# Kernel tuning notes

Measured on AMD Instinct MI355X. Metric: run time of the kernel, lower is better.

Reference implementation:

```python
import jax, jax.numpy as jnp
import numpy as np

N, E, H = 4096, 32768, 8
D0, C1, C2, C3 = 256, 448, 384, 256
K, M, G = 4, 500, 2000
NEG = 0.2   # GATConv LeakyReLU negative slope
EPS = 1e-5  # LayerNorm eps


def _gat(x, src, dst, W, a_s, a_d, b, heads, out_ch, concat):
    # PyG GATConv (self-loops already appended to src/dst by caller).
    n = x.shape[0]
    xp = (x @ W).reshape(n, heads, out_ch)                 # [N,H,C]
    s = jnp.einsum('nhc,hc->nh', xp, a_s)                  # alpha_src per node
    d = jnp.einsum('nhc,hc->nh', xp, a_d)                  # alpha_dst per node
    e = jax.nn.leaky_relu(s[src] + d[dst], NEG)            # [E,H]
    m = jax.ops.segment_max(e, dst, num_segments=n)
    m = jnp.where(jnp.isfinite(m), m, 0.0)
    p = jnp.exp(e - m[dst])
    z = jax.ops.segment_sum(p, dst, num_segments=n)
    alpha = p / (z[dst] + 1e-16)                           # per-dst softmax
    out = jax.ops.segment_sum(alpha[:, :, None] * xp[src], dst, num_segments=n)
    out = out.reshape(n, heads * out_ch) if concat else out[:, 0, :]
    return out + b


def _ln(x, g, b):
    mu = x.mean(-1, keepdims=True)
    v = ((x - mu) ** 2).mean(-1, keepdims=True)
    return (x - mu) * jax.lax.rsqrt(v + EPS) * g + b


def setup_inputs() -> dict:
    key = jax.random.key(0)
    ks = jax.random.split(key, 20)
    sc = 0.05
    inp = {
        'x': jax.random.normal(ks[0], (N, D0), jnp.float32),
        'edge_index': jax.random.randint(ks[1], (2, E), 0, N, jnp.int32),
        'W1': jax.random.normal(ks[2], (D0, H * C1), jnp.float32) * sc,
        'as1': jax.random.normal(ks[3], (H, C1), jnp.float32) * sc,
        'ad1': jax.random.normal(ks[4], (H, C1), jnp.float32) * sc,
        'b1': jnp.zeros((H * C1,), jnp.float32),
        'g1': jnp.ones((H * C1,), jnp.float32),
        'be1': jnp.zeros((H * C1,), jnp.float32),
        'W2': jax.random.normal(ks[5], (H * C1, H * C2), jnp.float32) * sc,
        'as2': jax.random.normal(ks[6], (H, C2), jnp.float32) * sc,
        'ad2': jax.random.normal(ks[7], (H, C2), jnp.float32) * sc,
        'b2': jnp.zeros((H * C2,), jnp.float32),
        'g2': jnp.ones((H * C2,), jnp.float32),
        'be2': jnp.zeros((H * C2,), jnp.float32),
        'W3': jax.random.normal(ks[8], (H * C2, H * C3), jnp.float32) * sc,
        'as3': jax.random.normal(ks[9], (H, C3), jnp.float32) * sc,
        'ad3': jax.random.normal(ks[10], (H, C3), jnp.float32) * sc,
        'b3': jnp.zeros((H * C3,), jnp.float32),
        'g3': jnp.ones((H * C3,), jnp.float32),
        'be3': jnp.zeros((H * C3,), jnp.float32),
        'Wh': jax.random.normal(ks[11], (K, H * C3, M), jnp.float32) * sc,
        'ash': jax.random.normal(ks[12], (K, 1, M), jnp.float32) * sc,
        'adh': jax.random.normal(ks[13], (K, 1, M), jnp.float32) * sc,
        'bh': jnp.zeros((K, M), jnp.float32),
        'idx': jnp.arange(G, dtype=jnp.int32).reshape(K, M),
    }
    return inp


def reference(x, edge_index, W1, as1, ad1, b1, g1, be1, W2, as2, ad2, b2, g2, be2,
              W3, as3, ad3, b3, g3, be3, Wh, ash, adh, bh, idx):
    n = x.shape[0]
    # eval mode: dropout_edge is identity; PyG GATConv adds self-loops
    loops = jnp.arange(n, dtype=edge_index.dtype)
    src = jnp.concatenate([edge_index[0], loops])
    dst = jnp.concatenate([edge_index[1], loops])

    h = jax.nn.relu(_gat(x, src, dst, W1, as1, ad1, b1, H, C1, True))
    h = _ln(h, g1, be1)
    h = jax.nn.relu(_gat(h, src, dst, W2, as2, ad2, b2, H, C2, True))
    h = _ln(h, g2, be2)
    h = jax.nn.relu(_gat(h, src, dst, W3, as3, ad3, b3, H, C3, True))
    h = _ln(h, g3, be3)

    per_head = jax.vmap(
        lambda Wk, ak_s, ak_d, bk: _gat(h, src, dst, Wk, ak_s, ak_d, bk, 1, M, False)
    )(Wh, ash, adh, bh)                                    # [K,N,M]

    vals = per_head.transpose(1, 0, 2).reshape(n, K * M)   # [N, G] in head order
    full = jnp.zeros((n, G), vals.dtype).at[:, idx.reshape(-1)].set(vals)
    return full, per_head
```

## Files before the change

### kernel.cpp

```cpp
#include <hip/hip_runtime.h>

#define NN 4096
#define EE 32768
#define ETOT (EE + NN)
#define HH 8
#define KK 4
#define MM 500
#define GG 2000
#define NEGS 0.2f
#define LNEPS 1e-5f

typedef unsigned short ushort;
typedef _Float16 half_t;
typedef __attribute__((ext_vector_type(8))) _Float16 half8;
typedef __attribute__((ext_vector_type(4))) _Float16 half4;
typedef __attribute__((ext_vector_type(4))) float floatx4;


__device__ __forceinline__ void get_edge(const int* __restrict__ ei, int e, int& s, int& d) {
    if (e < EE) { s = ei[e]; d = ei[EE + e]; }
    else        { s = e - EE; d = e - EE; }
}

__device__ __forceinline__ half_t f2h(float x) { return (half_t)x; }

__device__ __forceinline__ void async_lds16(const half_t* g, half_t* l) {
    __builtin_amdgcn_global_load_lds(
        (const __attribute__((address_space(1))) unsigned int*)(const void*)g,
        (__attribute__((address_space(3))) unsigned int*)(void*)l,
        16, 0, 0);
}


__global__ void k_count(const int* __restrict__ ei, int* deg) {
    int e = blockIdx.x * 256 + threadIdx.x;
    if (e < ETOT) { int s, d; get_edge(ei, e, s, d); atomicAdd(&deg[d], 1); }
}

__global__ void k_scan(int* deg, int* rs, int n) {
    __shared__ int sums[1024];
    int tid = threadIdx.x;
    int base = tid * 4;
    int loc[4]; int s = 0;
    #pragma unroll
    for (int i = 0; i < 4; i++) {
        int v = (base + i < n) ? deg[base + i] : 0;
        loc[i] = s; s += v;
    }
    #pragma unroll
    for (int i = 0; i < 4; i++)
        if (base + i < n) deg[base + i] = 0;
    sums[tid] = s;
    __syncthreads();
    for (int off = 1; off < 1024; off <<= 1) {
        int v = (tid >= off) ? sums[tid - off] : 0;
        __syncthreads();
        sums[tid] += v;
        __syncthreads();
    }
    int prev = (tid > 0) ? sums[tid - 1] : 0;
    #pragma unroll
    for (int i = 0; i < 4; i++)
        if (base + i < n) rs[base + i] = prev + loc[i];
    if (tid == 1023) rs[n] = sums[1023];
}

__global__ void k_fill_f2h(const int* __restrict__ ei, const int* __restrict__ rs,
                           int* cur, int* csr_src,
                           const floatx4* __restrict__ x4, half4* __restrict__ xh4) {
    int i = blockIdx.x * 256 + threadIdx.x;
    if (i < ETOT) {
        int s, d; get_edge(ei, i, s, d);
        int pos = rs[d] + atomicAdd(&cur[d], 1);
        csr_src[pos] = s;
    }
    if (i < NN * 64) {
        floatx4 v = x4[i];
        half4 o;
        o[0] = f2h(v[0]); o[1] = f2h(v[1]); o[2] = f2h(v[2]); o[3] = f2h(v[3]);
        xh4[i] = o;
    }
}


__global__ __launch_bounds__(256) void k_wa(const float* __restrict__ W1,
                                            const float* __restrict__ as_,
                                            const float* __restrict__ ad_,
                                            float* was, float* wad, int C, int ldw) {
    int pair = blockIdx.x * 4 + (threadIdx.x >> 6);
    int lane = threadIdx.x & 63;
    int h = pair >> 8, k = pair & 255;
    const float* wrow = W1 + (size_t)k * ldw + (size_t)h * C;
    const float* av = as_ + (size_t)h * C;
    const float* bv = ad_ + (size_t)h * C;
    float ss = 0.f, dd = 0.f;
    for (int c = lane; c < C; c += 64) {
        float w = wrow[c];
        ss += w * av[c];
        dd += w * bv[c];
    }
    #pragma unroll
    for (int o = 32; o > 0; o >>= 1) {
        ss += __shfl_down(ss, o, 64);
        dd += __shfl_down(dd, o, 64);
    }
    if (lane == 0) { was[pair] = ss; wad[pair] = dd; }
}


__global__ __launch_bounds__(256) void k_sd_x(const float* __restrict__ x,
                                              const float* __restrict__ was,
                                              const float* __restrict__ wad,
                                              float* s, float* d) {
    int n = blockIdx.x * 4 + (threadIdx.x >> 6);
    int lane = threadIdx.x & 63;
    const float* xr = x + (size_t)n * 256;
    float x0 = xr[lane], x1 = xr[lane + 64], x2 = xr[lane + 128], x3 = xr[lane + 192];
    #pragma unroll
    for (int h = 0; h < HH; h++) {
        const float* ws = was + h * 256;
        const float* wd = wad + h * 256;
        float ss = x0 * ws[lane] + x1 * ws[lane + 64] + x2 * ws[lane + 128] + x3 * ws[lane + 192];
        float dd = x0 * wd[lane] + x1 * wd[lane + 64] + x2 * wd[lane + 128] + x3 * wd[lane + 192];
        #pragma unroll
        for (int o = 32; o > 0; o >>= 1) {
            ss += __shfl_down(ss, o, 64);
            dd += __shfl_down(dd, o, 64);
        }
        if (lane == 0) { s[n * HH + h] = ss; d[n * HH + h] = dd; }
    }
}


__global__ __launch_bounds__(256) void k_agg_x(
    const half_t* __restrict__ xh, const float* __restrict__ s, const float* __restrict__ d,
    const int* __restrict__ csr_src, const int* __restrict__ rs,
    half_t* __restrict__ aggx) {
    __shared__ half_t sx[16][256];
    __shared__ int ssrc[16];
    __shared__ float sw[16][HH];
    __shared__ float sh_d[HH];
    __shared__ float sh_z[HH];
    int n = blockIdx.x, tid = threadIdx.x;
    int h = tid >> 5, kc = (tid & 31) * 8;
    if (tid < HH) { sh_d[tid] = d[(size_t)n * HH + tid]; sh_z[tid] = 0.f; }
    float acc[8];
    #pragma unroll
    for (int e = 0; e < 8; e++) acc[e] = 0.f;
    int start = rs[n], end = rs[n + 1];

    for (int e0 = start; e0 < end; e0 += 16) {
        int cnt = min(16, end - e0);
        if (tid < cnt) ssrc[tid] = csr_src[e0 + tid];
        __syncthreads();
        for (int q = tid; q < cnt * 32; q += 256) {
            int er = q >> 5, ec = q & 31;
            *((half8*)&sx[er][0] + ec) = *((const half8*)(xh + (size_t)ssrc[er] * 256) + ec);
        }
        if (tid < cnt * HH) {
            int er = tid >> 3, hh = tid & 7;
            float v = s[(size_t)ssrc[er] * HH + hh] + sh_d[hh];
            v = (v >= 0.f) ? v : NEGS * v;
            sw[er][hh] = expf(v);
        }
        __syncthreads();
        if (tid < HH) {
            float zz = 0.f;
            for (int i = 0; i < cnt; i++) zz += sw[i][tid];
            sh_z[tid] += zz;
        }
        for (int i = 0; i < cnt; i++) {
            float w = sw[i][h];
            half8 v = *(const half8*)&sx[i][kc];
            acc[0] += w * (float)v[0]; acc[1] += w * (float)v[1];
            acc[2] += w * (float)v[2]; acc[3] += w * (float)v[3];
            acc[4] += w * (float)v[4]; acc[5] += w * (float)v[5];
            acc[6] += w * (float)v[6]; acc[7] += w * (float)v[7];
        }
    }
    __syncthreads();
    float zi = 1.f / (sh_z[h] + 1e-16f);
    half8 o;
    #pragma unroll
    for (int e = 0; e < 8; e++) o[e] = f2h(acc[e] * zi);
    *(half8*)(aggx + (size_t)n * (HH * 256) + h * 256 + kc) = o;
}


__global__ __launch_bounds__(256) void k_ln(const half_t* __restrict__ xin,
                                            const float* __restrict__ bias,
                                            const float* __restrict__ gam,
                                            const float* __restrict__ bet,
                                            half_t* __restrict__ outh, int Dout) {
    __shared__ float red[256];
    __shared__ float red2[256];
    int n = blockIdx.x, tid = threadIdx.x;
    int NCH = Dout >> 3;
    float vals[2][8];
    float sum = 0.f, sumsq = 0.f;
    int ai = 0;
    for (int ch = tid; ch < NCH; ch += 256, ai++) {
        half8 v = *(const half8*)(xin + (size_t)n * Dout + (ch << 3));
        #pragma unroll
        for (int e = 0; e < 8; e++) {
            float val = (float)v[e] + bias[(ch << 3) + e];
            val = fmaxf(val, 0.f);
            vals[ai][e] = val;
            sum += val; sumsq += val * val;
        }
    }
    red[tid] = sum; red2[tid] = sumsq;
    __syncthreads();
    for (int o = 128; o > 0; o >>= 1) {
        if (tid < o) { red[tid] += red[tid + o]; red2[tid] += red2[tid + o]; }
        __syncthreads();
    }
    float mu = red[0] / Dout;
    float var = red2[0] / Dout - mu * mu;
    float rstd = rsqrtf(var + LNEPS);
    ai = 0;
    for (int ch = tid; ch < NCH; ch += 256, ai++) {
        half8 o;
        #pragma unroll
        for (int e = 0; e < 8; e++)
            o[e] = f2h((vals[ai][e] - mu) * rstd * gam[(ch << 3) + e] + bet[(ch << 3) + e]);
        *(half8*)(outh + (size_t)n * Dout + (ch << 3)) = o;
    }
}


__device__ __forceinline__ void sd_body(const half_t* __restrict__ xp,
                                        const float* __restrict__ as_,
                                        const float* __restrict__ ad_,
                                        float* s, float* d, int H, int C,
                                        int idx, int lane) {
    const half4* row4 = (const half4*)(xp + (size_t)idx * C);
    int h = idx % H;
    const float* av = as_ + (size_t)h * C;
    const float* bv = ad_ + (size_t)h * C;
    int C4 = C >> 2;
    float ss = 0.f, dd = 0.f;
    for (int c4 = lane; c4 < C4; c4 += 64) {
        half4 v = row4[c4];
        floatx4 a = *(const floatx4*)(av + c4 * 4);
        floatx4 b = *(const floatx4*)(bv + c4 * 4);
        float x0 = (float)v[0], x1 = (float)v[1], x2 = (float)v[2], x3 = (float)v[3];
        ss += x0 * a[0] + x1 * a[1] + x2 * a[2] + x3 * a[3];
        dd += x0 * b[0] + x1 * b[1] + x2 * b[2] + x3 * b[3];
    }
    #pragma unroll
    for (int o = 32; o > 0; o >>= 1) {
        ss += __shfl_down(ss, o, 64);
        dd += __shfl_down(dd, o, 64);
    }
    if (lane == 0) { s[idx] = ss; d[idx] = dd; }
}

__global__ __launch_bounds__(256) void k_sd4(const half_t* __restrict__ xp,
                                             const float* __restrict__ as_,
                                             const float* __restrict__ ad_,
                                             float* s, float* d, int H, int C, int npairs) {
    int idx = blockIdx.x * 4 + (threadIdx.x >> 6);
    if (idx < npairs)
        sd_body(xp, as_, ad_, s, d, H, C, idx, threadIdx.x & 63);
}


__global__ __launch_bounds__(256) void k_sd_wt(
    const half_t* __restrict__ xp, const float* __restrict__ as_,
    const float* __restrict__ ad_, float* s, float* d, int H, int C, int nsd, int npairs,
    const float* __restrict__ W, half_t* __restrict__ Wt,
    int Kd, int Nvalid, int ldw, long long sW, long long sWt, int wgx, int wgy) {
    __shared__ float t[32][33];
    int bid = blockIdx.x;
    if (bid < nsd) {
        int idx = bid * 4 + (threadIdx.x >> 6);
        if (idx < npairs)
            sd_body(xp, as_, ad_, s, d, H, C, idx, threadIdx.x & 63);
        return;
    }
    int wb = bid - nsd;
    int bx = wb % wgx;
    int rem = wb / wgx;
    int by = rem % wgy;
    int bz = rem / wgy;
    const float* Wp = W + (size_t)bz * sW;
    half_t* Wtp = Wt + (size_t)bz * sWt;
    int n0 = bx * 32, k0 = by * 32;
    int tx = threadIdx.x & 31, ty = threadIdx.x >> 5;
    #pragma unroll
    for (int i = 0; i < 32; i += 8)
        t[ty + i][tx] = (n0 + tx < Nvalid) ? Wp[(size_t)(k0 + ty + i) * ldw + n0 + tx] : 0.f;
    __syncthreads();
    #pragma unroll
    for (int i = 0; i < 32; i += 8)
        Wtp[(size_t)(n0 + ty + i) * Kd + k0 + tx] = f2h(t[tx][ty + i]);
}


__global__ __launch_bounds__(256) void k_wt(const float* __restrict__ W,
                                            half_t* __restrict__ Wt,
                                            int Kd, int Nvalid, int ldw,
                                            long long sW, long long sWt) {
    __shared__ float t[32][33];
    const float* Wp = W + (size_t)blockIdx.z * sW;
    half_t* Wtp = Wt + (size_t)blockIdx.z * sWt;
    int n0 = blockIdx.x * 32, k0 = blockIdx.y * 32;
    int tx = threadIdx.x & 31, ty = threadIdx.x >> 5;
    #pragma unroll
    for (int i = 0; i < 32; i += 8)
        t[ty + i][tx] = (n0 + tx < Nvalid) ? Wp[(size_t)(k0 + ty + i) * ldw + n0 + tx] : 0.f;
    __syncthreads();
    #pragma unroll
    for (int i = 0; i < 32; i += 8)
        Wtp[(size_t)(n0 + ty + i) * Kd + k0 + tx] = f2h(t[tx][ty + i]);
}


#define BM 128
#define BN 128
#define BK 64

__global__ __launch_bounds__(256) void k_gemm_mfma(
    const half_t* __restrict__ A,
    const half_t* __restrict__ Bt,
    half_t* __restrict__ C,
    int Kd, int lda, int Nreal, int ldc,
    long long strideA, long long strideBt, long long strideC)
{
    __shared__ __align__(16) half_t As[BM * BK];
    __shared__ __align__(16) half_t Bs[BN * BK];

    const half_t* Ap  = A  + (size_t)blockIdx.z * strideA;
    const half_t* Btp = Bt + (size_t)blockIdx.z * strideBt;
    half_t* Cp = C + (size_t)blockIdx.z * strideC;
    int col0 = blockIdx.x * BN, row0 = blockIdx.y * BM;

    int lane = threadIdx.x & 63;
    int wave = threadIdx.x >> 6;
    int wm = (wave >> 1) * 64, wn = (wave & 1) * 64;

    int srow = wave * 32 + (lane >> 3);
    int gchunk = (lane & 7) ^ ((lane >> 3) & 7);
    const half_t* ga = Ap  + (size_t)(row0 + srow) * lda + gchunk * 8;
    const half_t* gb = Btp + (size_t)(col0 + srow) * Kd + gchunk * 8;
    half_t* lA = &As[(wave * 32) * BK];
    half_t* lB = &Bs[(wave * 32) * BK];

    int r = lane & 15;
    int rx = r & 7;

    floatx4 acc[4][4];
    #pragma unroll
    for (int i = 0; i < 4; i++)
        #pragma unroll
        for (int j = 0; j < 4; j++) acc[i][j] = (floatx4){0.f, 0.f, 0.f, 0.f};

    for (int k0 = 0; k0 < Kd; k0 += BK) {
        #pragma unroll
        for (int j = 0; j < 4; j++) {
            async_lds16(ga + k0 + (size_t)(j * 8) * lda, lA + (j * 8) * BK);
            async_lds16(gb + k0 + (size_t)(j * 8) * Kd, lB + (j * 8) * BK);
        }
        __syncthreads();
        #pragma unroll
        for (int kk = 0; kk < BK; kk += 32) {
            int phys = (((kk >> 3) + (lane >> 4)) ^ rx) << 3;
            half8 a[4], b[4];
            #pragma unroll
            for (int i = 0; i < 4; i++)
                a[i] = *(const half8*)&As[(wm + i * 16 + r) * BK + phys];
            #pragma unroll
            for (int j = 0; j < 4; j++)
                b[j] = *(const half8*)&Bs[(wn + j * 16 + r) * BK + phys];
            #pragma unroll
            for (int i = 0; i < 4; i++)
                #pragma unroll
                for (int j = 0; j < 4; j++)
                    acc[i][j] = __builtin_amdgcn_mfma_f32_16x16x32_f16(a[i], b[j], acc[i][j], 0, 0, 0);
        }
        __syncthreads();
    }

    int q4 = (lane >> 4) * 4;
    #pragma unroll
    for (int i = 0; i < 4; i++) {
        #pragma unroll
        for (int rr = 0; rr < 4; rr++) {
            int row = row0 + wm + i * 16 + q4 + rr;
            #pragma unroll
            for (int j = 0; j < 4; j++) {
                int col = col0 + wn + j * 16 + (lane & 15);
                if (col < Nreal) Cp[(size_t)row * ldc + col] = f2h(acc[i][j][rr]);
            }
        }
    }
}


__global__ __launch_bounds__(256) void k_agg_ln(
    const half_t* __restrict__ xp, const float* __restrict__ s, const float* __restrict__ d,
    const int* __restrict__ csr_src, const int* __restrict__ rs,
    const float* __restrict__ bias, const float* __restrict__ gam,
    const float* __restrict__ bet, half_t* __restrict__ outh, int H, int C) {
    __shared__ int sh_src[256];
    __shared__ float sh_w[256 * HH];
    __shared__ float sh_d[HH];
    __shared__ float sh_z[HH];
    __shared__ float red[256];
    __shared__ float red2[256];
    int n = blockIdx.x, tid = threadIdx.x;
    int Dout = H * C;
    int NCH = Dout >> 3;
    int CCH = C >> 3;
    int start = rs[n], end = rs[n + 1];
    if (tid < H) { sh_d[tid] = d[(size_t)n * H + tid]; sh_z[tid] = 0.f; }
    float acc[2][8];
    #pragma unroll
    for (int a = 0; a < 2; a++)
        #pragma unroll
        for (int e = 0; e < 8; e++) acc[a][e] = 0.f;

    for (int e0 = start; e0 < end; e0 += 256) {
        int cnt = min(256, end - e0);
        if (tid < cnt) sh_src[tid] = csr_src[e0 + tid];
        __syncthreads();
        for (int i = tid; i < cnt * H; i += 256) {
            int ei = i / H, h = i - ei * H;
            float v = s[(size_t)sh_src[ei] * H + h] + sh_d[h];
            v = (v >= 0.f) ? v : NEGS * v;
            sh_w[i] = expf(v);
        }
        __syncthreads();
        if (tid < H) {
            float zz = 0.f;
            for (int i = 0; i < cnt; i++) zz += sh_w[i * H + tid];
            sh_z[tid] += zz;
        }
        int ai = 0;
        for (int ch = tid; ch < NCH; ch += 256, ai++) {
            int h = ch / CCH;
            float a0 = acc[ai][0], a1 = acc[ai][1], a2 = acc[ai][2], a3 = acc[ai][3];
            float a4 = acc[ai][4], a5 = acc[ai][5], a6 = acc[ai][6], a7 = acc[ai][7];
            for (int i = 0; i < cnt; i++) {
                float w = sh_w[i * H + h];
                half8 v = *(const half8*)(xp + (size_t)sh_src[i] * Dout + (ch << 3));
                a0 += w * (float)v[0]; a1 += w * (float)v[1];
                a2 += w * (float)v[2]; a3 += w * (float)v[3];
                a4 += w * (float)v[4]; a5 += w * (float)v[5];
                a6 += w * (float)v[6]; a7 += w * (float)v[7];
            }
            acc[ai][0] = a0; acc[ai][1] = a1; acc[ai][2] = a2; acc[ai][3] = a3;
            acc[ai][4] = a4; acc[ai][5] = a5; acc[ai][6] = a6; acc[ai][7] = a7;
        }
        __syncthreads();
    }

    float vals[2][8];
    float sum = 0.f, sumsq = 0.f;
    int ai = 0;
    for (int ch = tid; ch < NCH; ch += 256, ai++) {
        int h = ch / CCH;
        float zi = 1.f / (sh_z[h] + 1e-16f);
        #pragma unroll
        for (int e = 0; e < 8; e++) {
            float v = acc[ai][e] * zi + bias[(ch << 3) + e];
            v = fmaxf(v, 0.f);
            vals[ai][e] = v;
            sum += v; sumsq += v * v;
        }
    }
    red[tid] = sum; red2[tid] = sumsq;
    __syncthreads();
    for (int o = 128; o > 0; o >>= 1) {
        if (tid < o) { red[tid] += red[tid + o]; red2[tid] += red2[tid + o]; }
        __syncthreads();
    }
    float mu = red[0] / Dout;
    float var = red2[0] / Dout - mu * mu;
    float rstd = rsqrtf(var + LNEPS);
    ai = 0;
    for (int ch = tid; ch < NCH; ch += 256, ai++) {
        half8 o;
        #pragma unroll
        for (int e = 0; e < 8; e++)
            o[e] = f2h((vals[ai][e] - mu) * rstd * gam[(ch << 3) + e] + bet[(ch << 3) + e]);
        *(half8*)(outh + (size_t)n * Dout + (ch << 3)) = o;
    }
}


__global__ __launch_bounds__(256) void k_agg_head(
    const half_t* __restrict__ xp, const float* __restrict__ s, const float* __restrict__ d,
    const int* __restrict__ csr_src, const int* __restrict__ rs,
    const float* __restrict__ bias, const int* __restrict__ idxm,
    float* out_full, float* out_ph) {
    __shared__ int sh_src[256];
    __shared__ float sh_w[256 * KK];
    __shared__ float sh_d[KK];
    __shared__ float sh_z[KK];
    int n = blockIdx.x, tid = threadIdx.x;
    const int Dout = KK * MM;
    const int NCH = Dout >> 3;
    int start = rs[n], end = rs[n + 1];
    if (tid < KK) { sh_d[tid] = d[(size_t)n * KK + tid]; sh_z[tid] = 0.f; }
    float acc[8];
    #pragma unroll
    for (int e = 0; e < 8; e++) acc[e] = 0.f;
    int ch = tid;
    int cb = ch << 3;

    for (int e0 = start; e0 < end; e0 += 256) {
        int cnt = min(256, end - e0);
        if (tid < cnt) sh_src[tid] = csr_src[e0 + tid];
        __syncthreads();
        for (int i = tid; i < cnt * KK; i += 256) {
            int ei = i / KK, k = i - ei * KK;
            float v = s[(size_t)sh_src[ei] * KK + k] + sh_d[k];
            v = (v >= 0.f) ? v : NEGS * v;
            sh_w[i] = expf(v);
        }
        __syncthreads();
        if (tid < KK) {
            float zz = 0.f;
            for (int i = 0; i < cnt; i++) zz += sh_w[i * KK + tid];
            sh_z[tid] += zz;
        }
        if (ch < NCH) {
            for (int i = 0; i < cnt; i++) {
                const float* wv = &sh_w[i * KK];
                half8 v = *(const half8*)(xp + (size_t)sh_src[i] * Dout + cb);
                #pragma unroll
                for (int e = 0; e < 8; e++)
                    acc[e] += wv[(cb + e) / MM] * (float)v[e];
            }
        }
        __syncthreads();
    }
    if (ch < NCH) {
        #pragma unroll
        for (int e = 0; e < 8; e++) {
            int c = cb + e;
            int k = c / MM, m = c - k * MM;
            float v = acc[e] / (sh_z[k] + 1e-16f) + bias[c];
            out_ph[((size_t)k * NN + n) * MM + m] = v;
            out_full[(size_t)n * GG + idxm[c]] = v;
        }
    }
}


extern "C" void kernel_launch(void* const* d_in, const int* in_sizes, int n_in,
                              void* d_out, int out_size, void* d_ws, size_t ws_size,
                              hipStream_t stream) {
    (void)in_sizes; (void)n_in; (void)out_size; (void)ws_size;
    const float* x   = (const float*)d_in[0];
    const int*   ei  = (const int*)d_in[1];
    const float* W1  = (const float*)d_in[2];
    const float* as1 = (const float*)d_in[3];
    const float* ad1 = (const float*)d_in[4];
    const float* b1  = (const float*)d_in[5];
    const float* g1  = (const float*)d_in[6];
    const float* be1 = (const float*)d_in[7];
    const float* W2  = (const float*)d_in[8];
    const float* as2 = (const float*)d_in[9];
    const float* ad2 = (const float*)d_in[10];
    const float* b2  = (const float*)d_in[11];
    const float* g2  = (const float*)d_in[12];
    const float* be2 = (const float*)d_in[13];
    const float* W3  = (const float*)d_in[14];
    const float* as3 = (const float*)d_in[15];
    const float* ad3 = (const float*)d_in[16];
    const float* b3  = (const float*)d_in[17];
    const float* g3  = (const float*)d_in[18];
    const float* be3 = (const float*)d_in[19];
    const float* Wh  = (const float*)d_in[20];
    const float* ash = (const float*)d_in[21];
    const float* adh = (const float*)d_in[22];
    const float* bh  = (const float*)d_in[23];
    const int*   idxm = (const int*)d_in[24];
    float* out = (float*)d_out;

    char* w = (char*)d_ws;
    auto carve = [&](size_t bytes) { char* p = w; w += (bytes + 255) & ~(size_t)255; return p; };
    half_t* xp16    = (half_t*)carve((size_t)NN * 3584 * 2);
    half_t* Wt      = (half_t*)carve((size_t)12100000 * 2);
    float*  sarr    = (float*)carve((size_t)NN * HH * 4);
    float*  darr    = (float*)carve((size_t)NN * HH * 4);
    float*  was     = (float*)carve((size_t)HH * 256 * 4);
    float*  wad     = (float*)carve((size_t)HH * 256 * 4);
    int*    csr_src = (int*)carve((size_t)ETOT * 4);
    int*    rowst   = (int*)carve((size_t)(NN + 1) * 4);
    int*    cur     = (int*)carve((size_t)NN * 4);
    half_t* Ah   = (half_t*)d_out;
    half_t* aggx = (half_t*)(out + (size_t)NN * GG);
    half_t* Wt2  = Wt + (size_t)1048576;

    hipMemsetAsync(cur, 0, (size_t)NN * 4, stream);
    k_count<<<(ETOT + 255) / 256, 256, 0, stream>>>(ei, cur);
    k_scan<<<1, 1024, 0, stream>>>(cur, rowst, NN);
    k_fill_f2h<<<(NN * 64 + 255) / 256, 256, 0, stream>>>(
        ei, rowst, cur, csr_src, (const floatx4*)x, (half4*)Ah);

    k_wa<<<(HH * 256) / 4, 256, 0, stream>>>(W1, as1, ad1, was, wad, 448, 3584);
    k_wt<<<dim3(3584 / 32, 256 / 32, 1), 256, 0, stream>>>(W1, Wt, 256, 3584, 3584, 0, 0);
    k_sd_x<<<NN / 4, 256, 0, stream>>>(x, was, wad, sarr, darr);
    k_agg_x<<<NN, 256, 0, stream>>>(Ah, sarr, darr, csr_src, rowst, aggx);
    k_gemm_mfma<<<dim3(4, NN / BM, HH), 256, 0, stream>>>(
        aggx, Wt, xp16, 256, HH * 256, 448, 3584,
        256LL, (long long)448 * 256, 448LL);
    k_ln<<<NN, 256, 0, stream>>>(xp16, b1, g1, be1, Ah, 3584);

    k_wt<<<dim3(3072 / 32, 3584 / 32, 1), 256, 0, stream>>>(W2, Wt2, 3584, 3072, 3072, 0, 0);
    k_gemm_mfma<<<dim3(3072 / BN, NN / BM, 1), 256, 0, stream>>>(
        Ah, Wt2, xp16, 3584, 3584, 3072, 3072, 0, 0, 0);
    k_sd_wt<<<8192 + 6144, 256, 0, stream>>>(
        xp16, as2, ad2, sarr, darr, HH, 384, 8192, NN * HH,
        W3, Wt, 3072, 2048, 2048, 0, 0, 64, 96);
    k_agg_ln<<<NN, 256, 0, stream>>>(xp16, sarr, darr, csr_src, rowst,
                                     b2, g2, be2, Ah, HH, 384);

    k_gemm_mfma<<<dim3(2048 / BN, NN / BM, 1), 256, 0, stream>>>(
        Ah, Wt, xp16, 3072, 3072, 2048, 2048, 0, 0, 0);
    k_sd_wt<<<8192 + 4096, 256, 0, stream>>>(
        xp16, as3, ad3, sarr, darr, HH, 256, 8192, NN * HH,
        Wh, Wt, 2048, MM, MM, (long long)2048 * MM, (long long)512 * 2048, 16, 64);
    k_agg_ln<<<NN, 256, 0, stream>>>(xp16, sarr, darr, csr_src, rowst,
                                     b3, g3, be3, Ah, HH, 256);

    k_gemm_mfma<<<dim3(512 / BN, NN / BM, KK), 256, 0, stream>>>(
        Ah, Wt, xp16, 2048, 2048, MM, GG, 0, (long long)512 * 2048, (long long)MM);
    k_sd4<<<(NN * KK) / 4, 256, 0, stream>>>(xp16, ash, adh, sarr, darr, KK, MM, NN * KK);
    k_agg_head<<<NN, 256, 0, stream>>>(xp16, sarr, darr, csr_src, rowst,
                                       bh, idxm, out, out + (size_t)NN * GG);
}
```

Baseline: 644.9 us.

## Merge independent prologue kernels and add XCD-aware block swizzle to GEMM

Merges independent setup work into shared launches: the W1 attention-projection and W1 transpose now run in one kernel, the CSR fill/x conversion and the s/d projection share another, and the W2 transpose rides along with the first LayerNorm launch. This cuts launch count and lets independent blocks fill the GPU together. It also remaps GEMM block indices in groups of 8 so neighbouring tiles land on the same XCD, aiming to improve L2 reuse. One risk is that the s/d projection now runs after the CSR fill in the same launch, which adds a dependency on was/wad, although those are produced in the prior launch.

```diff
diff --git a/kernel.cpp b/kernel.cpp
--- a/kernel.cpp
+++ b/kernel.cpp
@@ -65,54 +65,72 @@
     if (tid == 1023) rs[n] = sums[1023];
 }
 
-__global__ void k_fill_f2h(const int* __restrict__ ei, const int* __restrict__ rs,
-                           int* cur, int* csr_src,
-                           const floatx4* __restrict__ x4, half4* __restrict__ xh4) {
-    int i = blockIdx.x * 256 + threadIdx.x;
-    if (i < ETOT) {
-        int s, d; get_edge(ei, i, s, d);
-        int pos = rs[d] + atomicAdd(&cur[d], 1);
-        csr_src[pos] = s;
-    }
-    if (i < NN * 64) {
-        floatx4 v = x4[i];
-        half4 o;
-        o[0] = f2h(v[0]); o[1] = f2h(v[1]); o[2] = f2h(v[2]); o[3] = f2h(v[3]);
-        xh4[i] = o;
-    }
-}
-
-
-__global__ __launch_bounds__(256) void k_wa(const float* __restrict__ W1,
-                                            const float* __restrict__ as_,
-                                            const float* __restrict__ ad_,
-                                            float* was, float* wad, int C, int ldw) {
-    int pair = blockIdx.x * 4 + (threadIdx.x >> 6);
-    int lane = threadIdx.x & 63;
-    int h = pair >> 8, k = pair & 255;
-    const float* wrow = W1 + (size_t)k * ldw + (size_t)h * C;
-    const float* av = as_ + (size_t)h * C;
-    const float* bv = ad_ + (size_t)h * C;
-    float ss = 0.f, dd = 0.f;
-    for (int c = lane; c < C; c += 64) {
-        float w = wrow[c];
-        ss += w * av[c];
-        dd += w * bv[c];
-    }
-    #pragma unroll
-    for (int o = 32; o > 0; o >>= 1) {
-        ss += __shfl_down(ss, o, 64);
-        dd += __shfl_down(dd, o, 64);
-    }
-    if (lane == 0) { was[pair] = ss; wad[pair] = dd; }
-}
-
-
-__global__ __launch_bounds__(256) void k_sd_x(const float* __restrict__ x,
-                                              const float* __restrict__ was,
-                                              const float* __restrict__ wad,
-                                              float* s, float* d) {
-    int n = blockIdx.x * 4 + (threadIdx.x >> 6);
+
+#define NWA 512
+#define WT1X 112
+__global__ __launch_bounds__(256) void k_wa_wt1(
+    const float* __restrict__ W1, const float* __restrict__ as_,
+    const float* __restrict__ ad_, float* was, float* wad,
+    half_t* __restrict__ Wt) {
+    __shared__ float t[32][33];
+    int bid = blockIdx.x;
+    if (bid < NWA) {
+        int pair = bid * 4 + (threadIdx.x >> 6);
+        int lane = threadIdx.x & 63;
+        int h = pair >> 8, k = pair & 255;
+        const float* wrow = W1 + (size_t)k * 3584 + (size_t)h * 448;
+        const float* av = as_ + (size_t)h * 448;
+        const float* bv = ad_ + (size_t)h * 448;
+        float ss = 0.f, dd = 0.f;
+        for (int c = lane; c < 448; c += 64) {
+            float w = wrow[c];
+            ss += w * av[c];
+            dd += w * bv[c];
+        }
+        #pragma unroll
+        for (int o = 32; o > 0; o >>= 1) {
+            ss += __shfl_down(ss, o, 64);
+            dd += __shfl_down(dd, o, 64);
+        }
+        if (lane == 0) { was[pair] = ss; wad[pair] = dd; }
+        return;
+    }
+    int wb = bid - NWA;
+    int bx = wb % WT1X, by = wb / WT1X;
+    int n0 = bx * 32, k0 = by * 32;
+    int tx = threadIdx.x & 31, ty = threadIdx.x >> 5;
+    #pragma unroll
+    for (int i = 0; i < 32; i += 8)
+        t[ty + i][tx] = W1[(size_t)(k0 + ty + i) * 3584 + n0 + tx];
+    __syncthreads();
+    #pragma unroll
+    for (int i = 0; i < 32; i += 8)
+        Wt[(size_t)(n0 + ty + i) * 256 + k0 + tx] = f2h(t[tx][ty + i]);
+}
+
+
+__global__ __launch_bounds__(256) void k_fill_f2h_sdx(
+    const int* __restrict__ ei, const int* __restrict__ rs, int* cur, int* csr_src,
+    const floatx4* __restrict__ x4, half4* __restrict__ xh4,
+    const float* __restrict__ x, const float* __restrict__ was,
+    const float* __restrict__ wad, float* s, float* d) {
+    int bid = blockIdx.x;
+    if (bid < 1024) {
+        int i = bid * 256 + threadIdx.x;
+        if (i < ETOT) {
+            int ss, dd; get_edge(ei, i, ss, dd);
+            int pos = rs[dd] + atomicAdd(&cur[dd], 1);
+            csr_src[pos] = ss;
+        }
+        if (i < NN * 64) {
+            floatx4 v = x4[i];
+            half4 o;
+            o[0] = f2h(v[0]); o[1] = f2h(v[1]); o[2] = f2h(v[2]); o[3] = f2h(v[3]);
+            xh4[i] = o;
+        }
+        return;
+    }
+    int n = (bid - 1024) * 4 + (threadIdx.x >> 6);
     int lane = threadIdx.x & 63;
     const float* xr = x + (size_t)n * 256;
     float x0 = xr[lane], x1 = xr[lane + 64], x2 = xr[lane + 128], x3 = xr[lane + 192];
@@ -187,15 +205,33 @@
 }
 
 
-__global__ __launch_bounds__(256) void k_ln(const half_t* __restrict__ xin,
-                                            const float* __restrict__ bias,
-                                            const float* __restrict__ gam,
-                                            const float* __restrict__ bet,
-                                            half_t* __restrict__ outh, int Dout) {
+#define WT2X 96
+__global__ __launch_bounds__(256) void k_ln_wt2(
+    const half_t* __restrict__ xin, const float* __restrict__ bias,
+    const float* __restrict__ gam, const float* __restrict__ bet,
+    half_t* __restrict__ outh,
+    const float* __restrict__ W2, half_t* __restrict__ Wt2) {
+    __shared__ float t[32][33];
     __shared__ float red[256];
     __shared__ float red2[256];
-    int n = blockIdx.x, tid = threadIdx.x;
-    int NCH = Dout >> 3;
+    int bid = blockIdx.x, tid = threadIdx.x;
+    if (bid >= NN) {
+        int wb = bid - NN;
+        int bx = wb % WT2X, by = wb / WT2X;
+        int n0 = bx * 32, k0 = by * 32;
+        int tx = tid & 31, ty = tid >> 5;
+        #pragma unroll
+        for (int i = 0; i < 32; i += 8)
+            t[ty + i][tx] = W2[(size_t)(k0 + ty + i) * 3072 + n0 + tx];
+        __syncthreads();
+        #pragma unroll
+        for (int i = 0; i < 32; i += 8)
+            Wt2[(size_t)(n0 + ty + i) * 3584 + k0 + tx] = f2h(t[tx][ty + i]);
+        return;
+    }
+    const int Dout = 3584;
+    const int NCH = Dout >> 3;
+    int n = bid;
     float vals[2][8];
     float sum = 0.f, sumsq = 0.f;
     int ai = 0;
@@ -298,25 +334,6 @@
 }
 
 
-__global__ __launch_bounds__(256) void k_wt(const float* __restrict__ W,
-                                            half_t* __restrict__ Wt,
-                                            int Kd, int Nvalid, int ldw,
-                                            long long sW, long long sWt) {
-    __shared__ float t[32][33];
-    const float* Wp = W + (size_t)blockIdx.z * sW;
-    half_t* Wtp = Wt + (size_t)blockIdx.z * sWt;
-    int n0 = blockIdx.x * 32, k0 = blockIdx.y * 32;
-    int tx = threadIdx.x & 31, ty = threadIdx.x >> 5;
-    #pragma unroll
-    for (int i = 0; i < 32; i += 8)
-        t[ty + i][tx] = (n0 + tx < Nvalid) ? Wp[(size_t)(k0 + ty + i) * ldw + n0 + tx] : 0.f;
-    __syncthreads();
-    #pragma unroll
-    for (int i = 0; i < 32; i += 8)
-        Wtp[(size_t)(n0 + ty + i) * Kd + k0 + tx] = f2h(t[tx][ty + i]);
-}
-
-
 #define BM 128
 #define BN 128
 #define BK 64
@@ -334,7 +351,17 @@
     const half_t* Ap  = A  + (size_t)blockIdx.z * strideA;
     const half_t* Btp = Bt + (size_t)blockIdx.z * strideBt;
     half_t* Cp = C + (size_t)blockIdx.z * strideC;
-    int col0 = blockIdx.x * BN, row0 = blockIdx.y * BM;
+
+    int bx = blockIdx.x, by = blockIdx.y;
+    int nb = gridDim.x * gridDim.y;
+    if ((nb & 7) == 0) {
+        int bid = by * gridDim.x + bx;
+        int nper = nb >> 3;
+        int swz = (bid & 7) * nper + (bid >> 3);
+        bx = swz % gridDim.x;
+        by = swz / gridDim.x;
+    }
+    int col0 = bx * BN, row0 = by * BM;
 
     int lane = threadIdx.x & 63;
     int wave = threadIdx.x >> 6;
@@ -599,19 +626,17 @@
     hipMemsetAsync(cur, 0, (size_t)NN * 4, stream);
     k_count<<<(ETOT + 255) / 256, 256, 0, stream>>>(ei, cur);
     k_scan<<<1, 1024, 0, stream>>>(cur, rowst, NN);
-    k_fill_f2h<<<(NN * 64 + 255) / 256, 256, 0, stream>>>(
-        ei, rowst, cur, csr_src, (const floatx4*)x, (half4*)Ah);
-
-    k_wa<<<(HH * 256) / 4, 256, 0, stream>>>(W1, as1, ad1, was, wad, 448, 3584);
-    k_wt<<<dim3(3584 / 32, 256 / 32, 1), 256, 0, stream>>>(W1, Wt, 256, 3584, 3584, 0, 0);
-    k_sd_x<<<NN / 4, 256, 0, stream>>>(x, was, wad, sarr, darr);
+    k_wa_wt1<<<NWA + WT1X * 8, 256, 0, stream>>>(W1, as1, ad1, was, wad, Wt);
+    k_fill_f2h_sdx<<<2048, 256, 0, stream>>>(
+        ei, rowst, cur, csr_src, (const floatx4*)x, (half4*)Ah,
+        x, was, wad, sarr, darr);
+
     k_agg_x<<<NN, 256, 0, stream>>>(Ah, sarr, darr, csr_src, rowst, aggx);
     k_gemm_mfma<<<dim3(4, NN / BM, HH), 256, 0, stream>>>(
         aggx, Wt, xp16, 256, HH * 256, 448, 3584,
         256LL, (long long)448 * 256, 448LL);
-    k_ln<<<NN, 256, 0, stream>>>(xp16, b1, g1, be1, Ah, 3584);
-
-    k_wt<<<dim3(3072 / 32, 3584 / 32, 1), 256, 0, stream>>>(W2, Wt2, 3584, 3072, 3072, 0, 0);
+    k_ln_wt2<<<NN + WT2X * 112, 256, 0, stream>>>(xp16, b1, g1, be1, Ah, W2, Wt2);
+
     k_gemm_mfma<<<dim3(3072 / BN, NN / BM, 1), 256, 0, stream>>>(
         Ah, Wt2, xp16, 3584, 3584, 3072, 3072, 0, 0, 0);
     k_sd_wt<<<8192 + 6144, 256, 0, stream>>>(
```

Measured after the change: 607.3 us. 1.06x faster.
